# Kernel tuning notes

Hardware: AMD Instinct MI355X
Metric: run time of the kernel (lower is better)

The kernel has to match this reference:

```python
import jax, jax.numpy as jnp
import numpy as np

N = 40000
E = 640000
D_IN = 128
D_H = 128
D_OUT = 1


def setup_inputs() -> dict:
    key = jax.random.key(0)
    ks = jax.random.split(key, 10)
    s = 1.0 / np.sqrt(D_IN)
    sh = 1.0 / np.sqrt(D_H)
    return {
        "x": jax.random.normal(ks[0], (N, D_IN), dtype=jnp.float32),
        "edge_index": jax.random.randint(ks[1], (2, E), 0, N, dtype=jnp.int64),
        # conv1: lin_l (neighbors, has bias), lin_r (root, no bias)
        "W1l": jax.random.uniform(ks[2], (D_IN, D_H), jnp.float32, -s, s),
        "b1": jnp.zeros((D_H,), jnp.float32),
        "W1r": jax.random.uniform(ks[3], (D_IN, D_H), jnp.float32, -s, s),
        # conv2
        "W2l": jax.random.uniform(ks[4], (D_H, D_H), jnp.float32, -sh, sh),
        "b2": jnp.zeros((D_H,), jnp.float32),
        "W2r": jax.random.uniform(ks[5], (D_H, D_H), jnp.float32, -sh, sh),
        # final linear
        "Wo": jax.random.uniform(ks[6], (D_H, D_OUT), jnp.float32, -sh, sh),
        "bo": jnp.zeros((D_OUT,), jnp.float32),
    }


def _mean_aggregate(x, src, dst, num_nodes):
    # mean over incoming edges per target node (PyG SAGEConv default aggr='mean')
    msg_sum = jax.ops.segment_sum(x[src], dst, num_segments=num_nodes)  # [N, D]
    deg = jax.ops.segment_sum(jnp.ones((src.shape[0],), x.dtype), dst,
                              num_segments=num_nodes)
    return msg_sum / jnp.maximum(deg, 1.0)[:, None]


def _sage_conv(x, src, dst, Wl, b, Wr):
    # out = lin_l(mean_agg(neighbors)) + lin_r(x)
    agg = _mean_aggregate(x, src, dst, x.shape[0])
    return agg @ Wl + b + x @ Wr


def reference(x, edge_index, W1l, b1, W1r, W2l, b2, W2r, Wo, bo):
    src, dst = edge_index[0], edge_index[1]
    h = jax.nn.relu(_sage_conv(x, src, dst, W1l, b1, W1r))
    h = jax.nn.relu(_sage_conv(h, src, dst, W2l, b2, W2r))
    return h @ Wo + bo
```

## Files before the change

### kernel.cpp

```cpp
#include <hip/hip_runtime.h>
#include <hip/hip_bf16.h>


#define DH 128
#define CAP 64
#define BCAP 160

typedef __attribute__((ext_vector_type(8))) short bf16x8;
typedef __attribute__((ext_vector_type(4))) float f32x4;

__device__ __forceinline__ unsigned short f2bf_rne(float f) {
    unsigned int u = __float_as_uint(f);
    return (unsigned short)((u + 0x7FFFu + ((u >> 16) & 1u)) >> 16);
}
__device__ __forceinline__ float bf2f(unsigned short h) {
    return __uint_as_float(((unsigned int)h) << 16);
}
__device__ __forceinline__ float bflo(unsigned int u) {
    return __uint_as_float(u << 16);
}
__device__ __forceinline__ float bfhi(unsigned int u) {
    return __uint_as_float(u & 0xffff0000u);
}
__device__ __forceinline__ unsigned packpair_hi(float a, float b) {
    return (__float_as_uint(b) & 0xffff0000u) | (__float_as_uint(a) >> 16);
}
__device__ __forceinline__ unsigned packpair_lo(float a, float b) {
    float ra = a - bfhi(__float_as_uint(a));
    float rb = b - bfhi(__float_as_uint(b));
    return ((unsigned)f2bf_rne(rb) << 16) | f2bf_rne(ra);
}


__global__ __launch_bounds__(256) void prep_kernel(
    const float* __restrict__ x,
    unsigned short* __restrict__ xhi, unsigned short* __restrict__ xlo,
    const int* __restrict__ src, const int* __restrict__ dst,
    int* __restrict__ bcur, unsigned* __restrict__ buckets,
    const float* __restrict__ W1l, const float* __restrict__ W1r,
    const float* __restrict__ W2l, const float* __restrict__ W2r,
    unsigned short* __restrict__ whi, unsigned short* __restrict__ wlo,
    int n4, int E, int nbA, int nbB, int nRanges)
{
    int b = blockIdx.x;
    if (b < nbB) {
        int e = b * 256 + threadIdx.x;
        if (e >= E) return;
        unsigned xcc;
        asm volatile("s_getreg_b32 %0, hwreg(HW_REG_XCC_ID)" : "=s"(xcc));
        xcc &= 7;
        int d = dst[e];
        int s = src[e];
        int range = d >> 5;
        int pos = atomicAdd(&bcur[((int)xcc * nRanges + range) * 16], 1);
        if (pos < BCAP)
            buckets[((size_t)range * 8 + xcc) * BCAP + pos] =
                ((unsigned)(d & 31) << 16) | (unsigned)s;
    } else if (b < nbB + nbA) {
        int i = (b - nbB) * 256 + threadIdx.x;
        if (i >= n4) return;
        float4 v = ((const float4*)x)[i];
        unsigned short hx = f2bf_rne(v.x), hy = f2bf_rne(v.y);
        unsigned short hz = f2bf_rne(v.z), hw = f2bf_rne(v.w);
        uint2 hi, lo;
        hi.x = ((unsigned)hy << 16) | hx;
        hi.y = ((unsigned)hw << 16) | hz;
        lo.x = ((unsigned)f2bf_rne(v.y - bf2f(hy)) << 16) | f2bf_rne(v.x - bf2f(hx));
        lo.y = ((unsigned)f2bf_rne(v.w - bf2f(hw)) << 16) | f2bf_rne(v.z - bf2f(hz));
        ((uint2*)xhi)[i] = hi;
        ((uint2*)xlo)[i] = lo;
    } else {
        int tid = (b - nbB - nbA) * 256 + threadIdx.x;
        if (tid >= 2 * 8 * 8 * 64) return;
        int lane = tid & 63;
        int f = (tid >> 6) & 7;
        int t = (tid >> 9) & 7;
        int conv = tid >> 12;
        const float* Wl = conv ? W2l : W1l;
        const float* Wr = conv ? W2r : W1r;
        int c = f * 16 + (lane & 15);
        int kb = t * 32 + (lane >> 4) * 8;
        size_t off = (size_t)tid * 8;
        #pragma unroll
        for (int j = 0; j < 8; ++j) {
            int k = kb + j;
            float w = (k < 128) ? Wl[k * 128 + c] : Wr[(k - 128) * 128 + c];
            unsigned short h = f2bf_rne(w);
            whi[off + j] = h;
            wlo[off + j] = f2bf_rne(w - bf2f(h));
        }
    }
}


__global__ __launch_bounds__(512) void gather_demux_kernel(
    const unsigned short* __restrict__ featbf,
    const unsigned* __restrict__ buckets, const int* __restrict__ bcur,
    unsigned short* __restrict__ outhi, unsigned short* __restrict__ outlo,
    int nRanges)
{
    __shared__ unsigned short csr_lds[32 * CAP];
    __shared__ int cnt[32];
    const int blk = blockIdx.x;
    const int tid = threadIdx.x;
    if (tid < 32) cnt[tid] = 0;
    __syncthreads();
    #pragma unroll
    for (int s = 0; s < 8; ++s) {
        int c = min(bcur[(s * nRanges + blk) * 16], BCAP);
        const unsigned* bp = buckets + ((size_t)blk * 8 + s) * BCAP;
        for (int i = tid; i < c; i += 512) {
            unsigned p = bp[i];
            int dlow = p >> 16;
            int pos = atomicAdd(&cnt[dlow], 1);
            if (pos < CAP)
                csr_lds[dlow * CAP + pos] = (unsigned short)(p & 0xffffu);
        }
    }
    __syncthreads();

    const int lane = tid & 63;
    const int wv = tid >> 6;
    const int ch = lane & 7;
    const int slot = lane >> 3;

    for (int i = 0; i < 4; ++i) {
        const int nlocal = wv * 4 + i;
        const int node = blk * 32 + nlocal;
        const int dg = min(cnt[nlocal], CAP);
        const unsigned short* row = &csr_lds[nlocal * CAP];

        float a[16], b[16];
        #pragma unroll
        for (int j = 0; j < 16; ++j) { a[j] = 0.f; b[j] = 0.f; }

        int e = slot;
        for (; e + 8 < dg; e += 16) {
            int s0 = row[e];
            int s1 = row[e + 8];
            const uint4* p0 = (const uint4*)&featbf[(size_t)s0 * DH + ch * 16];
            const uint4* p1 = (const uint4*)&featbf[(size_t)s1 * DH + ch * 16];
            uint4 v0 = p0[0], w0 = p0[1];
            uint4 v1 = p1[0], w1 = p1[1];
            a[0] += bflo(v0.x); a[1] += bfhi(v0.x); a[2] += bflo(v0.y); a[3] += bfhi(v0.y);
            a[4] += bflo(v0.z); a[5] += bfhi(v0.z); a[6] += bflo(v0.w); a[7] += bfhi(v0.w);
            a[8] += bflo(w0.x); a[9] += bfhi(w0.x); a[10]+= bflo(w0.y); a[11]+= bfhi(w0.y);
            a[12]+= bflo(w0.z); a[13]+= bfhi(w0.z); a[14]+= bflo(w0.w); a[15]+= bfhi(w0.w);
            b[0] += bflo(v1.x); b[1] += bfhi(v1.x); b[2] += bflo(v1.y); b[3] += bfhi(v1.y);
            b[4] += bflo(v1.z); b[5] += bfhi(v1.z); b[6] += bflo(v1.w); b[7] += bfhi(v1.w);
            b[8] += bflo(w1.x); b[9] += bfhi(w1.x); b[10]+= bflo(w1.y); b[11]+= bfhi(w1.y);
            b[12]+= bflo(w1.z); b[13]+= bfhi(w1.z); b[14]+= bflo(w1.w); b[15]+= bfhi(w1.w);
        }
        if (e < dg) {
            int s0 = row[e];
            const uint4* p0 = (const uint4*)&featbf[(size_t)s0 * DH + ch * 16];
            uint4 v0 = p0[0], w0 = p0[1];
            a[0] += bflo(v0.x); a[1] += bfhi(v0.x); a[2] += bflo(v0.y); a[3] += bfhi(v0.y);
            a[4] += bflo(v0.z); a[5] += bfhi(v0.z); a[6] += bflo(v0.w); a[7] += bfhi(v0.w);
            a[8] += bflo(w0.x); a[9] += bfhi(w0.x); a[10]+= bflo(w0.y); a[11]+= bfhi(w0.y);
            a[12]+= bflo(w0.z); a[13]+= bfhi(w0.z); a[14]+= bflo(w0.w); a[15]+= bfhi(w0.w);
        }
        #pragma unroll
        for (int j = 0; j < 16; ++j) a[j] += b[j];
        #pragma unroll
        for (int m = 8; m < 64; m <<= 1)
            #pragma unroll
            for (int j = 0; j < 16; ++j)
                a[j] += __shfl_xor(a[j], m);

        if (slot == 0) {
            float sc = 1.0f / (float)max(dg, 1);
            #pragma unroll
            for (int j = 0; j < 16; ++j) a[j] *= sc;
            uint4 hi0, hi1, lo0, lo1;
            hi0.x = packpair_hi(a[0], a[1]);   lo0.x = packpair_lo(a[0], a[1]);
            hi0.y = packpair_hi(a[2], a[3]);   lo0.y = packpair_lo(a[2], a[3]);
            hi0.z = packpair_hi(a[4], a[5]);   lo0.z = packpair_lo(a[4], a[5]);
            hi0.w = packpair_hi(a[6], a[7]);   lo0.w = packpair_lo(a[6], a[7]);
            hi1.x = packpair_hi(a[8], a[9]);   lo1.x = packpair_lo(a[8], a[9]);
            hi1.y = packpair_hi(a[10], a[11]); lo1.y = packpair_lo(a[10], a[11]);
            hi1.z = packpair_hi(a[12], a[13]); lo1.z = packpair_lo(a[12], a[13]);
            hi1.w = packpair_hi(a[14], a[15]); lo1.w = packpair_lo(a[14], a[15]);
            uint4* ph = (uint4*)&outhi[(size_t)node * DH + ch * 16];
            uint4* pl = (uint4*)&outlo[(size_t)node * DH + ch * 16];
            ph[0] = hi0; ph[1] = hi1;
            pl[0] = lo0; pl[1] = lo1;
        }
    }
}


template<int HEAD>
__global__ __launch_bounds__(256) void sage_mfma_kernel(
    const unsigned short* __restrict__ agghi, const unsigned short* __restrict__ agglo,
    const unsigned short* __restrict__ xhi, const unsigned short* __restrict__ xlo,
    const unsigned short* __restrict__ whi, const unsigned short* __restrict__ wlo,
    const float* __restrict__ bias,
    unsigned short* __restrict__ Hhi, unsigned short* __restrict__ Hlo,
    const float* __restrict__ Wo, const float* __restrict__ bo,
    float* __restrict__ outp, int N)
{
    const int l = threadIdx.x & 63;
    const int wv = threadIdx.x >> 6;
    const int r = l & 15;
    const int kq = l >> 4;
    const int base0 = blockIdx.x * 128 + wv * 16;
    const int base1 = base0 + 64;
    const bool v1 = (base1 + 16 <= N);

    f32x4 acc0[8], acc1[8];
    #pragma unroll
    for (int f = 0; f < 8; ++f) {
        float b = bias[f * 16 + r];
        acc0[f] = (f32x4){b, b, b, b};
        acc1[f] = (f32x4){b, b, b, b};
    }

    #pragma unroll
    for (int t = 0; t < 8; ++t) {
        const unsigned short* Ah = (t < 4) ? agghi : xhi;
        const unsigned short* Al = (t < 4) ? agglo : xlo;
        size_t ao0 = (size_t)(base0 + r) * DH + (t & 3) * 32 + kq * 8;
        bf16x8 a0h = *(const bf16x8*)&Ah[ao0];
        bf16x8 a0l = *(const bf16x8*)&Al[ao0];
        bf16x8 a1h = {0,0,0,0,0,0,0,0};
        bf16x8 a1l = {0,0,0,0,0,0,0,0};
        if (v1) {
            size_t ao1 = ao0 + (size_t)64 * DH;
            a1h = *(const bf16x8*)&Ah[ao1];
            a1l = *(const bf16x8*)&Al[ao1];
        }
        const unsigned short* bh = whi + ((size_t)(t * 8) * 64 + l) * 8;
        const unsigned short* bl = wlo + ((size_t)(t * 8) * 64 + l) * 8;
        #pragma unroll
        for (int f = 0; f < 8; ++f) {
            bf16x8 bhi = *(const bf16x8*)(bh + (size_t)f * 512);
            bf16x8 blo = *(const bf16x8*)(bl + (size_t)f * 512);
            acc0[f] = __builtin_amdgcn_mfma_f32_16x16x32_bf16(a0h, bhi, acc0[f], 0, 0, 0);
            acc0[f] = __builtin_amdgcn_mfma_f32_16x16x32_bf16(a0l, bhi, acc0[f], 0, 0, 0);
            acc0[f] = __builtin_amdgcn_mfma_f32_16x16x32_bf16(a0h, blo, acc0[f], 0, 0, 0);
            acc1[f] = __builtin_amdgcn_mfma_f32_16x16x32_bf16(a1h, bhi, acc1[f], 0, 0, 0);
            acc1[f] = __builtin_amdgcn_mfma_f32_16x16x32_bf16(a1l, bhi, acc1[f], 0, 0, 0);
            acc1[f] = __builtin_amdgcn_mfma_f32_16x16x32_bf16(a1h, blo, acc1[f], 0, 0, 0);
        }
    }

    if (HEAD == 0) {
        #pragma unroll
        for (int rg = 0; rg < 2; ++rg) {
            if (rg == 1 && !v1) break;
            int base = rg ? base1 : base0;
            #pragma unroll
            for (int f = 0; f < 8; ++f) {
                int col = f * 16 + r;
                #pragma unroll
                for (int q = 0; q < 4; ++q) {
                    float v = fmaxf(rg ? acc1[f][q] : acc0[f][q], 0.0f);
                    size_t idx = (size_t)(base + kq * 4 + q) * DH + col;
                    unsigned short h = f2bf_rne(v);
                    Hhi[idx] = h;
                    Hlo[idx] = f2bf_rne(v - bf2f(h));
                }
            }
        }
    } else {
        float wo[8];
        #pragma unroll
        for (int f = 0; f < 8; ++f) wo[f] = Wo[f * 16 + r];
        #pragma unroll
        for (int rg = 0; rg < 2; ++rg) {
            if (rg == 1 && !v1) break;
            int base = rg ? base1 : base0;
            float s[4] = {0.f, 0.f, 0.f, 0.f};
            #pragma unroll
            for (int f = 0; f < 8; ++f)
                #pragma unroll
                for (int q = 0; q < 4; ++q)
                    s[q] += fmaxf(rg ? acc1[f][q] : acc0[f][q], 0.0f) * wo[f];
            #pragma unroll
            for (int m = 1; m < 16; m <<= 1) {
                s[0] += __shfl_xor(s[0], m);
                s[1] += __shfl_xor(s[1], m);
                s[2] += __shfl_xor(s[2], m);
                s[3] += __shfl_xor(s[3], m);
            }
            if (r < 4) outp[base + kq * 4 + r] = s[r] + bo[0];
        }
    }
}

extern "C" void kernel_launch(void* const* d_in, const int* in_sizes, int n_in,
                              void* d_out, int out_size, void* d_ws, size_t ws_size,
                              hipStream_t stream) {
    const float* x   = (const float*)d_in[0];
    const int*   ei  = (const int*)d_in[1];
    const float* W1l = (const float*)d_in[2];
    const float* b1  = (const float*)d_in[3];
    const float* W1r = (const float*)d_in[4];
    const float* W2l = (const float*)d_in[5];
    const float* b2  = (const float*)d_in[6];
    const float* W2r = (const float*)d_in[7];
    const float* Wo  = (const float*)d_in[8];
    const float* bo  = (const float*)d_in[9];
    float* out = (float*)d_out;

    const int N = in_sizes[0] / DH;
    const int E = in_sizes[1] / 2;
    const int* src = ei;
    const int* dst = ei + E;
    const size_t NDH = (size_t)N * DH;
    const int n4 = N * DH / 4;
    const int nbA = (n4 + 255) / 256;
    const int nbB = (E + 255) / 256;
    const int nRanges = N / 32;

    unsigned short* xhi   = (unsigned short*)d_ws;
    unsigned short* xlo   = xhi + NDH;
    unsigned short* h1hi  = xlo + NDH;
    unsigned short* h1lo  = h1hi + NDH;
    unsigned short* agghi = h1lo + NDH;
    unsigned short* agglo = agghi + NDH;
    unsigned short* whi   = agglo + NDH;
    unsigned short* wlo   = whi + 65536;
    int* bcur = (int*)(wlo + 65536);
    unsigned* buckets = (unsigned*)(bcur + (size_t)nRanges * 8 * 16);

    hipMemsetAsync(bcur, 0, (size_t)nRanges * 8 * 16 * sizeof(int), stream);
    prep_kernel<<<nbA + nbB + 32, 256, 0, stream>>>(
        x, xhi, xlo, src, dst, bcur, buckets,
        W1l, W1r, W2l, W2r, whi, wlo, n4, E, nbA, nbB, nRanges);

    const int convGrid = (N + 127) / 128;

    gather_demux_kernel<<<nRanges, 512, 0, stream>>>(
        xhi, buckets, bcur, agghi, agglo, nRanges);
    sage_mfma_kernel<0><<<convGrid, 256, 0, stream>>>(
        agghi, agglo, xhi, xlo, whi, wlo, b1, h1hi, h1lo,
        nullptr, nullptr, nullptr, N);

    gather_demux_kernel<<<nRanges, 512, 0, stream>>>(
        h1hi, buckets, bcur, agghi, agglo, nRanges);
    sage_mfma_kernel<1><<<convGrid, 256, 0, stream>>>(
        agghi, agglo, h1hi, h1lo, whi + 32768, wlo + 32768, b2, nullptr, nullptr,
        Wo, bo, out, N);
}
```

Baseline: 237.7 us.

## Transform features before aggregation and fuse combine/ReLU/head into gather

Uses the linearity of mean aggregation to apply the weight matrices first: one GEMM produces x@Wl and x@Wr+b as bf16, and the gather then averages the projected neighbor rows, adds the root term, applies ReLU and writes the next layer (or the final Wo dot product). This removes the separate agg-then-GEMM pass and the hi/lo storage of the aggregate, and folds the output head into the second gather. The projected features are rounded to single bf16 instead of hi/lo pairs, which lowers accuracy. The GEMM grid assumes N is a multiple of 64.

```diff
diff --git a/kernel.cpp b/kernel.cpp
--- a/kernel.cpp
+++ b/kernel.cpp
@@ -71,10 +71,10 @@
         ((uint2*)xlo)[i] = lo;
     } else {
         int tid = (b - nbB - nbA) * 256 + threadIdx.x;
-        if (tid >= 2 * 8 * 8 * 64) return;
+        if (tid >= 2 * 4 * 16 * 64) return;
         int lane = tid & 63;
-        int f = (tid >> 6) & 7;
-        int t = (tid >> 9) & 7;
+        int f = (tid >> 6) & 15;
+        int t = (tid >> 10) & 3;
         int conv = tid >> 12;
         const float* Wl = conv ? W2l : W1l;
         const float* Wr = conv ? W2r : W1r;
@@ -84,7 +84,7 @@
         #pragma unroll
         for (int j = 0; j < 8; ++j) {
             int k = kb + j;
-            float w = (k < 128) ? Wl[k * 128 + c] : Wr[(k - 128) * 128 + c];
+            float w = (c < 128) ? Wl[k * 128 + c] : Wr[k * 128 + (c - 128)];
             unsigned short h = f2bf_rne(w);
             whi[off + j] = h;
             wlo[off + j] = f2bf_rne(w - bf2f(h));
@@ -93,11 +93,64 @@
 }
 
 
+__global__ __launch_bounds__(256) void gemm_kernel(
+    const unsigned short* __restrict__ Ahi, const unsigned short* __restrict__ Alo,
+    const unsigned short* __restrict__ whi, const unsigned short* __restrict__ wlo,
+    const float* __restrict__ bias,
+    unsigned short* __restrict__ o1, unsigned short* __restrict__ o2)
+{
+    const int l = threadIdx.x & 63;
+    const int wv = threadIdx.x >> 6;
+    const int r = l & 15;
+    const int kq = l >> 4;
+    const int base = blockIdx.x * 64 + wv * 16;
+
+    f32x4 acc[16];
+    #pragma unroll
+    for (int f = 0; f < 16; ++f) acc[f] = (f32x4){0.f, 0.f, 0.f, 0.f};
+
+    #pragma unroll
+    for (int t = 0; t < 4; ++t) {
+        size_t ao = (size_t)(base + r) * DH + t * 32 + kq * 8;
+        bf16x8 ah = *(const bf16x8*)&Ahi[ao];
+        bf16x8 al = *(const bf16x8*)&Alo[ao];
+        const unsigned short* bh = whi + ((size_t)(t * 16) * 64 + l) * 8;
+        const unsigned short* bl = wlo + ((size_t)(t * 16) * 64 + l) * 8;
+        #pragma unroll
+        for (int f = 0; f < 16; ++f) {
+            bf16x8 bhi = *(const bf16x8*)(bh + (size_t)f * 512);
+            bf16x8 blo = *(const bf16x8*)(bl + (size_t)f * 512);
+            acc[f] = __builtin_amdgcn_mfma_f32_16x16x32_bf16(ah, bhi, acc[f], 0, 0, 0);
+            acc[f] = __builtin_amdgcn_mfma_f32_16x16x32_bf16(al, bhi, acc[f], 0, 0, 0);
+            acc[f] = __builtin_amdgcn_mfma_f32_16x16x32_bf16(ah, blo, acc[f], 0, 0, 0);
+        }
+    }
+
+    float bv[8];
+    #pragma unroll
+    for (int j = 0; j < 8; ++j) bv[j] = bias[j * 16 + r];
+
+    #pragma unroll
+    for (int f = 0; f < 8; ++f) {
+        int col = f * 16 + r;
+        #pragma unroll
+        for (int q = 0; q < 4; ++q) {
+            int row = base + kq * 4 + q;
+            o1[(size_t)row * DH + col] = f2bf_rne(acc[f][q]);
+            o2[(size_t)row * DH + col] = f2bf_rne(acc[f + 8][q] + bv[f]);
+        }
+    }
+}
+
+
+template<int HEAD>
 __global__ __launch_bounds__(512) void gather_demux_kernel(
     const unsigned short* __restrict__ featbf,
     const unsigned* __restrict__ buckets, const int* __restrict__ bcur,
+    const unsigned short* __restrict__ addv,
     unsigned short* __restrict__ outhi, unsigned short* __restrict__ outlo,
-    int nRanges)
+    const float* __restrict__ Wo, const float* __restrict__ bo,
+    float* __restrict__ outp, int nRanges)
 {
     __shared__ unsigned short csr_lds[32 * CAP];
     __shared__ int cnt[32];
@@ -170,121 +223,44 @@
 
         if (slot == 0) {
             float sc = 1.0f / (float)max(dg, 1);
+            const uint4* ap = (const uint4*)&addv[(size_t)node * DH + ch * 16];
+            uint4 av0 = ap[0], av1 = ap[1];
+            float ad[16] = {
+                bflo(av0.x), bfhi(av0.x), bflo(av0.y), bfhi(av0.y),
+                bflo(av0.z), bfhi(av0.z), bflo(av0.w), bfhi(av0.w),
+                bflo(av1.x), bfhi(av1.x), bflo(av1.y), bfhi(av1.y),
+                bflo(av1.z), bfhi(av1.z), bflo(av1.w), bfhi(av1.w)};
             #pragma unroll
-            for (int j = 0; j < 16; ++j) a[j] *= sc;
-            uint4 hi0, hi1, lo0, lo1;
-            hi0.x = packpair_hi(a[0], a[1]);   lo0.x = packpair_lo(a[0], a[1]);
-            hi0.y = packpair_hi(a[2], a[3]);   lo0.y = packpair_lo(a[2], a[3]);
-            hi0.z = packpair_hi(a[4], a[5]);   lo0.z = packpair_lo(a[4], a[5]);
-            hi0.w = packpair_hi(a[6], a[7]);   lo0.w = packpair_lo(a[6], a[7]);
-            hi1.x = packpair_hi(a[8], a[9]);   lo1.x = packpair_lo(a[8], a[9]);
-            hi1.y = packpair_hi(a[10], a[11]); lo1.y = packpair_lo(a[10], a[11]);
-            hi1.z = packpair_hi(a[12], a[13]); lo1.z = packpair_lo(a[12], a[13]);
-            hi1.w = packpair_hi(a[14], a[15]); lo1.w = packpair_lo(a[14], a[15]);
-            uint4* ph = (uint4*)&outhi[(size_t)node * DH + ch * 16];
-            uint4* pl = (uint4*)&outlo[(size_t)node * DH + ch * 16];
-            ph[0] = hi0; ph[1] = hi1;
-            pl[0] = lo0; pl[1] = lo1;
-        }
-    }
-}
-
-
-template<int HEAD>
-__global__ __launch_bounds__(256) void sage_mfma_kernel(
-    const unsigned short* __restrict__ agghi, const unsigned short* __restrict__ agglo,
-    const unsigned short* __restrict__ xhi, const unsigned short* __restrict__ xlo,
-    const unsigned short* __restrict__ whi, const unsigned short* __restrict__ wlo,
-    const float* __restrict__ bias,
-    unsigned short* __restrict__ Hhi, unsigned short* __restrict__ Hlo,
-    const float* __restrict__ Wo, const float* __restrict__ bo,
-    float* __restrict__ outp, int N)
-{
-    const int l = threadIdx.x & 63;
-    const int wv = threadIdx.x >> 6;
-    const int r = l & 15;
-    const int kq = l >> 4;
-    const int base0 = blockIdx.x * 128 + wv * 16;
-    const int base1 = base0 + 64;
-    const bool v1 = (base1 + 16 <= N);
-
-    f32x4 acc0[8], acc1[8];
-    #pragma unroll
-    for (int f = 0; f < 8; ++f) {
-        float b = bias[f * 16 + r];
-        acc0[f] = (f32x4){b, b, b, b};
-        acc1[f] = (f32x4){b, b, b, b};
-    }
-
-    #pragma unroll
-    for (int t = 0; t < 8; ++t) {
-        const unsigned short* Ah = (t < 4) ? agghi : xhi;
-        const unsigned short* Al = (t < 4) ? agglo : xlo;
-        size_t ao0 = (size_t)(base0 + r) * DH + (t & 3) * 32 + kq * 8;
-        bf16x8 a0h = *(const bf16x8*)&Ah[ao0];
-        bf16x8 a0l = *(const bf16x8*)&Al[ao0];
-        bf16x8 a1h = {0,0,0,0,0,0,0,0};
-        bf16x8 a1l = {0,0,0,0,0,0,0,0};
-        if (v1) {
-            size_t ao1 = ao0 + (size_t)64 * DH;
-            a1h = *(const bf16x8*)&Ah[ao1];
-            a1l = *(const bf16x8*)&Al[ao1];
-        }
-        const unsigned short* bh = whi + ((size_t)(t * 8) * 64 + l) * 8;
-        const unsigned short* bl = wlo + ((size_t)(t * 8) * 64 + l) * 8;
-        #pragma unroll
-        for (int f = 0; f < 8; ++f) {
-            bf16x8 bhi = *(const bf16x8*)(bh + (size_t)f * 512);
-            bf16x8 blo = *(const bf16x8*)(bl + (size_t)f * 512);
-            acc0[f] = __builtin_amdgcn_mfma_f32_16x16x32_bf16(a0h, bhi, acc0[f], 0, 0, 0);
-            acc0[f] = __builtin_amdgcn_mfma_f32_16x16x32_bf16(a0l, bhi, acc0[f], 0, 0, 0);
-            acc0[f] = __builtin_amdgcn_mfma_f32_16x16x32_bf16(a0h, blo, acc0[f], 0, 0, 0);
-            acc1[f] = __builtin_amdgcn_mfma_f32_16x16x32_bf16(a1h, bhi, acc1[f], 0, 0, 0);
-            acc1[f] = __builtin_amdgcn_mfma_f32_16x16x32_bf16(a1l, bhi, acc1[f], 0, 0, 0);
-            acc1[f] = __builtin_amdgcn_mfma_f32_16x16x32_bf16(a1h, blo, acc1[f], 0, 0, 0);
-        }
-    }
-
-    if (HEAD == 0) {
-        #pragma unroll
-        for (int rg = 0; rg < 2; ++rg) {
-            if (rg == 1 && !v1) break;
-            int base = rg ? base1 : base0;
-            #pragma unroll
-            for (int f = 0; f < 8; ++f) {
-                int col = f * 16 + r;
-                #pragma unroll
-                for (int q = 0; q < 4; ++q) {
-                    float v = fmaxf(rg ? acc1[f][q] : acc0[f][q], 0.0f);
-                    size_t idx = (size_t)(base + kq * 4 + q) * DH + col;
-                    unsigned short h = f2bf_rne(v);
-                    Hhi[idx] = h;
-                    Hlo[idx] = f2bf_rne(v - bf2f(h));
-                }
+            for (int j = 0; j < 16; ++j)
+                a[j] = fmaxf(a[j] * sc + ad[j], 0.0f);
+
+            if (HEAD == 0) {
+                uint4 hi0, hi1, lo0, lo1;
+                hi0.x = packpair_hi(a[0], a[1]);   lo0.x = packpair_lo(a[0], a[1]);
+                hi0.y = packpair_hi(a[2], a[3]);   lo0.y = packpair_lo(a[2], a[3]);
+                hi0.z = packpair_hi(a[4], a[5]);   lo0.z = packpair_lo(a[4], a[5]);
+                hi0.w = packpair_hi(a[6], a[7]);   lo0.w = packpair_lo(a[6], a[7]);
+                hi1.x = packpair_hi(a[8], a[9]);   lo1.x = packpair_lo(a[8], a[9]);
+                hi1.y = packpair_hi(a[10], a[11]); lo1.y = packpair_lo(a[10], a[11]);
+                hi1.z = packpair_hi(a[12], a[13]); lo1.z = packpair_lo(a[12], a[13]);
+                hi1.w = packpair_hi(a[14], a[15]); lo1.w = packpair_lo(a[14], a[15]);
+                uint4* ph = (uint4*)&outhi[(size_t)node * DH + ch * 16];
+                uint4* pl = (uint4*)&outlo[(size_t)node * DH + ch * 16];
+                ph[0] = hi0; ph[1] = hi1;
+                pl[0] = lo0; pl[1] = lo1;
+            } else {
+                const float4* wp = (const float4*)&Wo[ch * 16];
+                float4 w0 = wp[0], w1 = wp[1], w2 = wp[2], w3 = wp[3];
+                float s =
+                    a[0]*w0.x + a[1]*w0.y + a[2]*w0.z + a[3]*w0.w +
+                    a[4]*w1.x + a[5]*w1.y + a[6]*w1.z + a[7]*w1.w +
+                    a[8]*w2.x + a[9]*w2.y + a[10]*w2.z + a[11]*w2.w +
+                    a[12]*w3.x + a[13]*w3.y + a[14]*w3.z + a[15]*w3.w;
+                s += __shfl_xor(s, 1);
+                s += __shfl_xor(s, 2);
+                s += __shfl_xor(s, 4);
+                if (ch == 0) outp[node] = s + bo[0];
             }
-        }
-    } else {
-        float wo[8];
-        #pragma unroll
-        for (int f = 0; f < 8; ++f) wo[f] = Wo[f * 16 + r];
-        #pragma unroll
-        for (int rg = 0; rg < 2; ++rg) {
-            if (rg == 1 && !v1) break;
-            int base = rg ? base1 : base0;
-            float s[4] = {0.f, 0.f, 0.f, 0.f};
-            #pragma unroll
-            for (int f = 0; f < 8; ++f)
-                #pragma unroll
-                for (int q = 0; q < 4; ++q)
-                    s[q] += fmaxf(rg ? acc1[f][q] : acc0[f][q], 0.0f) * wo[f];
-            #pragma unroll
-            for (int m = 1; m < 16; m <<= 1) {
-                s[0] += __shfl_xor(s[0], m);
-                s[1] += __shfl_xor(s[1], m);
-                s[2] += __shfl_xor(s[2], m);
-                s[3] += __shfl_xor(s[3], m);
-            }
-            if (r < 4) outp[base + kq * 4 + r] = s[r] + bo[0];
         }
     }
 }
@@ -314,14 +290,16 @@
     const int nbB = (E + 255) / 256;
     const int nRanges = N / 32;
 
-    unsigned short* xhi   = (unsigned short*)d_ws;
-    unsigned short* xlo   = xhi + NDH;
-    unsigned short* h1hi  = xlo + NDH;
-    unsigned short* h1lo  = h1hi + NDH;
-    unsigned short* agghi = h1lo + NDH;
-    unsigned short* agglo = agghi + NDH;
-    unsigned short* whi   = agglo + NDH;
-    unsigned short* wlo   = whi + 65536;
+    unsigned short* xhi  = (unsigned short*)d_ws;
+    unsigned short* xlo  = xhi + NDH;
+    unsigned short* h1hi = xlo + NDH;
+    unsigned short* h1lo = h1hi + NDH;
+    unsigned short* xl   = h1lo + NDH;
+    unsigned short* xr   = xl + NDH;
+    unsigned short* y1   = xr + NDH;
+    unsigned short* y2   = y1 + NDH;
+    unsigned short* whi  = y2 + NDH;
+    unsigned short* wlo  = whi + 65536;
     int* bcur = (int*)(wlo + 65536);
     unsigned* buckets = (unsigned*)(bcur + (size_t)nRanges * 8 * 16);
 
@@ -330,17 +308,14 @@
         x, xhi, xlo, src, dst, bcur, buckets,
         W1l, W1r, W2l, W2r, whi, wlo, n4, E, nbA, nbB, nRanges);
 
-    const int convGrid = (N + 127) / 128;
-
-    gather_demux_kernel<<<nRanges, 512, 0, stream>>>(
-        xhi, buckets, bcur, agghi, agglo, nRanges);
-    sage_mfma_kernel<0><<<convGrid, 256, 0, stream>>>(
-        agghi, agglo, xhi, xlo, whi, wlo, b1, h1hi, h1lo,
-        nullptr, nullptr, nullptr, N);
-
-    gather_demux_kernel<<<nRanges, 512, 0, stream>>>(
-        h1hi, buckets, bcur, agghi, agglo, nRanges);
-    sage_mfma_kernel<1><<<convGrid, 256, 0, stream>>>(
-        agghi, agglo, h1hi, h1lo, whi + 32768, wlo + 32768, b2, nullptr, nullptr,
-        Wo, bo, out, N);
-}
+    const int gemmGrid = N / 64;
+
+    gemm_kernel<<<gemmGrid, 256, 0, stream>>>(xhi, xlo, whi, wlo, b1, xl, xr);
+    gather_demux_kernel<0><<<nRanges, 512, 0, stream>>>(
+        xl, buckets, bcur, xr, h1hi, h1lo, nullptr, nullptr, nullptr, nRanges);
+
+    gemm_kernel<<<gemmGrid, 256, 0, stream>>>(h1hi, h1lo, whi + 32768, wlo + 32768,
+                                              b2, y1, y2);
+    gather_demux_kernel<1><<<nRanges, 512, 0, stream>>>(
+        y1, buckets, bcur, y2, nullptr, nullptr, Wo, bo, out, nRanges);
+}
```

New measurement: 237.9 us. Within noise of the previous version (+0.1%).
